# Kernel optimization log

Measured on AMD Instinct MI355X. Metric: run time of the kernel, lower is better.

Reference implementation:

```python
import jax, jax.numpy as jnp
import numpy as np

B, N, F_IN, F_HID, F_OUT = 32, 1024, 512, 512, 512


def setup_inputs() -> dict:
    key = jax.random.key(0)
    ks = jax.random.split(key, 8)
    def xavier(k, fan_in, fan_out):
        bound = float(np.sqrt(6.0 / (fan_in + fan_out)))
        return jax.random.uniform(k, (fan_in, fan_out), jnp.float32, -bound, bound)
    return {
        "batch_graph": jax.random.normal(ks[0], (B, N, F_IN), jnp.float32),
        "adj": jax.random.uniform(ks[1], (B, N, N), jnp.float32),
        "W1": xavier(ks[2], F_IN, F_HID),
        "b1": jnp.zeros((F_HID,), jnp.float32),
        "W2": xavier(ks[3], F_HID, F_HID),
        "b2": jnp.zeros((F_HID,), jnp.float32),
        "W3": xavier(ks[4], F_HID, F_OUT),
        "b3": jnp.zeros((F_OUT,), jnp.float32),
    }


def _gcn_layer(x, adj, W, b):
    # support = X @ W ; out = A @ support + b  (per graph in the batch)
    support = jnp.einsum("bnf,fh->bnh", x, W)
    return jnp.einsum("bnm,bmh->bnh", adj, support) + b


def reference(batch_graph, adj, W1, b1, W2, b2, W3, b3):
    # Block-diagonal big_adj @ big_graph is exactly a batched per-graph matmul:
    # the zero off-diagonal blocks contribute nothing, so math is identical.
    # Dropout is identity at inference (eval mode).
    x = jax.nn.relu(_gcn_layer(batch_graph, adj, W1, b1))
    x = jax.nn.relu(_gcn_layer(x, adj, W2, b2))
    out = _gcn_layer(x, adj, W3, b3)  # [B, N, F_OUT]
    return out
```

## Files before the change

### kernel.cpp

```cpp
#include <hip/hip_runtime.h>
#include <hip/hip_bf16.h>


typedef __attribute__((ext_vector_type(8))) short bf16x8s;
typedef __attribute__((ext_vector_type(4))) float f32x4;
typedef __attribute__((ext_vector_type(4))) unsigned short us4;
typedef __attribute__((ext_vector_type(8))) unsigned short us8;

__device__ __forceinline__ unsigned short f2bf(float f) {
    unsigned u = __builtin_bit_cast(unsigned, f);
    u += 0x7fffu + ((u >> 16) & 1u);
    return (unsigned short)(u >> 16);
}

__device__ __forceinline__ void async16(const unsigned short* g, unsigned short* l) {
    __builtin_amdgcn_global_load_lds(
        (const __attribute__((address_space(1))) unsigned int*)g,
        (__attribute__((address_space(3))) unsigned int*)l, 16, 0, 0);
}

#define MFMA_(d, va, vb) d = __builtin_amdgcn_mfma_f32_16x16x32_bf16(va, vb, d, 0, 0, 0)

__global__ void prep(const float* __restrict__ x0, unsigned short* __restrict__ P0, long n4,
                     const float* __restrict__ W1, const float* __restrict__ W2,
                     const float* __restrict__ W3, unsigned short* __restrict__ WT1,
                     unsigned short* __restrict__ WT2, unsigned short* __restrict__ WT3,
                     int F) {
    long i = (long)blockIdx.x * blockDim.x + threadIdx.x;
    long stride = (long)gridDim.x * blockDim.x;
    for (long k = i; k < n4; k += stride) {
        float4 v = ((const float4*)x0)[k];
        us4 o;
        o.x = f2bf(v.x); o.y = f2bf(v.y); o.z = f2bf(v.z); o.w = f2bf(v.w);
        ((us4*)P0)[k] = o;
    }
    const long FF = (long)F * F;
    for (long k = i; k < 3 * FF; k += stride) {
        int w = (int)(k / FF);
        long idx = k % FF;
        int r = (int)(idx % F);
        int c = (int)(idx / F);
        const float* W = (w == 0) ? W1 : (w == 1) ? W2 : W3;
        unsigned short* WT = (w == 0) ? WT1 : (w == 1) ? WT2 : WT3;
        WT[idx] = f2bf(W[(size_t)r * F + c]);
    }
}

template<bool RELU, bool OUT_F32, bool CVTTAIL>
__global__ __launch_bounds__(512, 2)
void gemm256(const unsigned short* __restrict__ A,
             const unsigned short* __restrict__ BT,
             void* __restrict__ Cout,
             const float* __restrict__ bias,
             int M, int N, int K,
             long sA, long sBT, long sC,
             const float* __restrict__ adjf,
             unsigned short* __restrict__ adjb)
{
    __shared__ unsigned short Lraw[65536];

    const int t    = threadIdx.x;
    const int lane = t & 63;
    const int wv   = t >> 6;
    const int wm   = wv >> 2;
    const int wn   = wv & 3;
    const int fr   = lane & 15;
    const int fk   = (lane >> 4) * 8;
    const int r4   = (lane >> 4) * 4;

    const int tilesN = N >> 8;
    const int bpb    = (M >> 8) * tilesN;
    const int cpx = gridDim.x >> 3;
    const int lb  = (blockIdx.x & 7) * cpx + (blockIdx.x >> 3);
    const int bat = lb / bpb;
    const int tt  = lb % bpb;
    const int m0  = (tt / tilesN) << 8;
    const int n0  = (tt % tilesN) << 8;

    const unsigned short* Ab = A  + (size_t)bat * sA  + (size_t)m0 * K;
    const unsigned short* Bb = BT + (size_t)bat * sBT + (size_t)n0 * K;

    int srow[2], scol[2], lo[2];
#pragma unroll
    for (int r = 0; r < 2; ++r) {
        int c   = r * 512 + t;
        srow[r] = c >> 3;
        scol[r] = ((c & 7) * 8) ^ ((srow[r] & 7) << 3);
        lo[r]   = c * 8;
    }

    auto stageA = [&](int kt, int h) {
        unsigned short* base = Lraw + (kt & 1) * 16384;
#pragma unroll
        for (int r = 0; r < 2; ++r)
            async16(Ab + (size_t)(h * 128 + srow[r]) * K + kt * 64 + scol[r],
                    base + h * 8192 + lo[r]);
    };
    auto stageB = [&](int kt, int h) {
        unsigned short* base = Lraw + 32768 + (kt & 1) * 16384;
#pragma unroll
        for (int r = 0; r < 2; ++r)
            async16(Bb + (size_t)(h * 128 + srow[r]) * K + kt * 64 + scol[r],
                    base + h * 8192 + lo[r]);
    };
    auto rdA = [&](int buf, int mf, int kkj) -> bf16x8s {
        int row = wm * 128 + mf * 16 + fr;
        int e   = (kkj * 32 + fk) ^ ((row & 7) << 3);
        return *(const bf16x8s*)&Lraw[buf * 16384 + row * 64 + e];
    };
    auto rdB = [&](int buf, int nf, int kkj) -> bf16x8s {
        int row = wn * 64 + nf * 16 + fr;
        int e   = (kkj * 32 + fk) ^ ((row & 7) << 3);
        return *(const bf16x8s*)&Lraw[32768 + buf * 16384 + row * 64 + e];
    };

    const int nt = K >> 6;

    f32x4 acc[8][4];
#pragma unroll
    for (int i = 0; i < 8; ++i)
#pragma unroll
        for (int j = 0; j < 4; ++j) acc[i][j] = f32x4{0.f, 0.f, 0.f, 0.f};

    bf16x8s aP[4], aB[4], aC[4], bX[4], bY[4];

    stageA(0, 0); stageB(0, 0); stageA(0, 1); stageB(0, 1);
    asm volatile("s_waitcnt vmcnt(0)" ::: "memory");
    __builtin_amdgcn_s_barrier();
#pragma unroll
    for (int m = 0; m < 4; ++m) aP[m] = rdA(0, m, 0);
#pragma unroll
    for (int n = 0; n < 4; ++n) bX[n] = rdB(0, n, 0);

    for (int it = 0; it < nt; ++it) {
        const int cur  = it & 1;
        const int nxt  = cur ^ 1;
        const bool more = (it + 1 < nt);

        __builtin_amdgcn_s_barrier();
#pragma unroll
        for (int m = 0; m < 4; ++m) aB[m] = rdA(cur, m + 4, 0);
        if (more) { stageA(it + 1, 0); stageB(it + 1, 0); }
        __builtin_amdgcn_s_setprio(1);
#pragma unroll
        for (int m = 0; m < 4; ++m)
#pragma unroll
            for (int n = 0; n < 4; ++n) MFMA_(acc[m][n], aP[m], bX[n]);
        __builtin_amdgcn_s_setprio(0);

        __builtin_amdgcn_s_barrier();
#pragma unroll
        for (int m = 0; m < 4; ++m) aC[m] = rdA(cur, m, 1);
#pragma unroll
        for (int n = 0; n < 4; ++n) bY[n] = rdB(cur, n, 1);
        if (more) { stageA(it + 1, 1); stageB(it + 1, 1); }
        __builtin_amdgcn_s_setprio(1);
#pragma unroll
        for (int m = 0; m < 4; ++m)
#pragma unroll
            for (int n = 0; n < 4; ++n) MFMA_(acc[m + 4][n], aB[m], bX[n]);
        __builtin_amdgcn_s_setprio(0);

        __builtin_amdgcn_s_barrier();
#pragma unroll
        for (int m = 0; m < 4; ++m) aB[m] = rdA(cur, m + 4, 1);
        __builtin_amdgcn_s_setprio(1);
#pragma unroll
        for (int m = 0; m < 4; ++m)
#pragma unroll
            for (int n = 0; n < 4; ++n) MFMA_(acc[m][n], aC[m], bY[n]);
        __builtin_amdgcn_s_setprio(0);

        if (more) {
            asm volatile("s_waitcnt vmcnt(0)" ::: "memory");
            __builtin_amdgcn_s_barrier();
#pragma unroll
            for (int m = 0; m < 4; ++m) aP[m] = rdA(nxt, m, 0);
#pragma unroll
            for (int n = 0; n < 4; ++n) bX[n] = rdB(nxt, n, 0);
        }
        __builtin_amdgcn_s_setprio(1);
#pragma unroll
        for (int m = 0; m < 4; ++m)
#pragma unroll
            for (int n = 0; n < 4; ++n) MFMA_(acc[m + 4][n], aB[m], bY[n]);
        __builtin_amdgcn_s_setprio(0);
    }

    __syncthreads();

    const int R0 = m0 + wm * 128;
    const int C0 = n0 + wn * 64;
    float bv[4];
#pragma unroll
    for (int j = 0; j < 4; ++j)
        bv[j] = bias ? bias[C0 + j * 16 + fr] : 0.f;

    if (OUT_F32) {
        float* Cb = (float*)Cout + (size_t)bat * sC;
#pragma unroll
        for (int j = 0; j < 4; ++j)
#pragma unroll
            for (int i = 0; i < 8; ++i)
#pragma unroll
                for (int e = 0; e < 4; ++e) {
                    float v = acc[i][j][e] + bv[j];
                    if (RELU) v = fmaxf(v, 0.f);
                    Cb[(size_t)(R0 + i * 16 + r4 + e) * N + C0 + j * 16 + fr] = v;
                }
    } else {
        unsigned short* sl = Lraw + wv * 8192;
#pragma unroll
        for (int i = 0; i < 8; ++i)
#pragma unroll
            for (int j = 0; j < 4; ++j)
#pragma unroll
                for (int e = 0; e < 4; ++e) {
                    float v = acc[i][j][e] + bv[j];
                    if (RELU) v = fmaxf(v, 0.f);
                    const int row = i * 16 + r4 + e;
                    const int col = j * 16 + fr;
                    sl[row * 64 + (col ^ ((row & 7) << 3))] = f2bf(v);
                }
        unsigned short* Cb = (unsigned short*)Cout + (size_t)bat * sC;
#pragma unroll
        for (int rr = 0; rr < 16; ++rr) {
            const int row = rr * 8 + (lane >> 3);
            const int k8  = lane & 7;
            us8 v = *(const us8*)&sl[row * 64 + ((k8 ^ (row & 7)) << 3)];
            *(us8*)&Cb[(size_t)(R0 + row) * N + C0 + k8 * 8] = v;
        }
    }

    if constexpr (CVTTAIL) {
        const int bc = lb >> 3, s = lb & 7;
        const float4* src = (const float4*)adjf + ((size_t)bc * 262144 + (size_t)s * 32768);
        us4* dst = (us4*)adjb + ((size_t)bc * 262144 + (size_t)s * 32768);
        for (int i = t; i < 32768; i += 512) {
            float4 v = src[i];
            us4 o;
            o.x = f2bf(v.x); o.y = f2bf(v.y); o.z = f2bf(v.z); o.w = f2bf(v.w);
            dst[i] = o;
        }
    }
}

extern "C" void kernel_launch(void* const* d_in, const int* in_sizes, int n_in,
                              void* d_out, int out_size, void* d_ws, size_t ws_size,
                              hipStream_t stream) {
    constexpr int B = 32, N = 1024, F = 512;

    const float* x0f  = (const float*)d_in[0];
    const float* adjf = (const float*)d_in[1];
    const float* W1 = (const float*)d_in[2];
    const float* b1 = (const float*)d_in[3];
    const float* W2 = (const float*)d_in[4];
    const float* b2 = (const float*)d_in[5];
    const float* W3 = (const float*)d_in[6];
    const float* b3 = (const float*)d_in[7];

    unsigned short* ws   = (unsigned short*)d_ws;
    unsigned short* adjb = ws;
    unsigned short* P0   = adjb + (size_t)B * N * N;
    unsigned short* P1   = P0 + (size_t)B * N * F;
    unsigned short* PT   = P1 + (size_t)B * N * F;
    unsigned short* WT1  = PT + (size_t)B * N * F;
    unsigned short* WT2  = WT1 + (size_t)F * F;
    unsigned short* WT3  = WT2 + (size_t)F * F;

    prep<<<2048, 256, 0, stream>>>(x0f, P0, (long)B * N * F / 4,
                                   W1, W2, W3, WT1, WT2, WT3, F);

    const int grid = 256;
    const long sX = (long)N * F;
    const long sAd = (long)N * N;

    gemm256<false, false, true ><<<grid, 512, 0, stream>>>(WT1,  P0, PT, nullptr, F, N, F, 0,  sX, sX, adjf, adjb);
    gemm256<true,  false, false><<<grid, 512, 0, stream>>>(adjb, PT, P1, b1,      N, F, N, sAd, sX, sX, nullptr, nullptr);
    gemm256<false, false, false><<<grid, 512, 0, stream>>>(WT2,  P1, PT, nullptr, F, N, F, 0,  sX, sX, nullptr, nullptr);
    gemm256<true,  false, false><<<grid, 512, 0, stream>>>(adjb, PT, P0, b2,      N, F, N, sAd, sX, sX, nullptr, nullptr);
    gemm256<false, false, false><<<grid, 512, 0, stream>>>(WT3,  P0, PT, nullptr, F, N, F, 0,  sX, sX, nullptr, nullptr);
    gemm256<false, true,  false><<<grid, 512, 0, stream>>>(adjb, PT, (float*)d_out, b3, N, F, N, sAd, sX, sX, nullptr, nullptr);
}
```

Measured before the change: 264.3 us.

## Overlap adjacency fp32-to-bf16 conversion with first GEMM using dedicated extra waves

The first feature GEMM launches 640 threads: two extra waves convert the adjacency matrix to bf16 in chunks interleaved with the GEMM's barrier phases, instead of all threads doing it after the epilogue. The aim is to hide the large conversion traffic behind the MFMA main loop. The cost is lower occupancy for this kernel, since launch bounds drop to one block per CU, and extra memory traffic competing with the GEMM's tile loads.

```diff
diff --git a/kernel.cpp b/kernel.cpp
--- a/kernel.cpp
+++ b/kernel.cpp
@@ -46,8 +46,8 @@
     }
 }
 
-template<bool RELU, bool OUT_F32, bool CVTTAIL>
-__global__ __launch_bounds__(512, 2)
+template<bool RELU, bool OUT_F32, bool CVTW>
+__global__ __launch_bounds__(CVTW ? 640 : 512, CVTW ? 1 : 2)
 void gemm256(const unsigned short* __restrict__ A,
              const unsigned short* __restrict__ BT,
              void* __restrict__ Cout,
@@ -62,6 +62,7 @@
     const int t    = threadIdx.x;
     const int lane = t & 63;
     const int wv   = t >> 6;
+    const bool isCvt = CVTW && (t >= 512);
     const int wm   = wv >> 2;
     const int wn   = wv & 3;
     const int fr   = lane & 15;
@@ -83,7 +84,7 @@
     int srow[2], scol[2], lo[2];
 #pragma unroll
     for (int r = 0; r < 2; ++r) {
-        int c   = r * 512 + t;
+        int c   = r * 512 + (t & 511);
         srow[r] = c >> 3;
         scol[r] = ((c & 7) * 8) ^ ((srow[r] & 7) << 3);
         lo[r]   = c * 8;
@@ -114,6 +115,22 @@
         return *(const bf16x8s*)&Lraw[32768 + buf * 16384 + row * 64 + e];
     };
 
+    auto cvtChunk = [&](int c) {
+        if constexpr (CVTW) {
+            const long base = (long)(lb >> 3) * 262144 + (long)(lb & 7) * 32768
+                            + (long)(wv - 8) * 16384 + (long)c * 512 + lane;
+            const float4* src = (const float4*)adjf;
+            us4* dst = (us4*)adjb;
+#pragma unroll
+            for (int k = 0; k < 8; ++k) {
+                float4 v = src[base + k * 64];
+                us4 o;
+                o.x = f2bf(v.x); o.y = f2bf(v.y); o.z = f2bf(v.z); o.w = f2bf(v.w);
+                dst[base + k * 64] = o;
+            }
+        }
+    };
+
     const int nt = K >> 6;
 
     f32x4 acc[8][4];
@@ -124,13 +141,17 @@
 
     bf16x8s aP[4], aB[4], aC[4], bX[4], bY[4];
 
-    stageA(0, 0); stageB(0, 0); stageA(0, 1); stageB(0, 1);
-    asm volatile("s_waitcnt vmcnt(0)" ::: "memory");
+    if (!isCvt) {
+        stageA(0, 0); stageB(0, 0); stageA(0, 1); stageB(0, 1);
+        asm volatile("s_waitcnt vmcnt(0)" ::: "memory");
+    }
     __builtin_amdgcn_s_barrier();
-#pragma unroll
-    for (int m = 0; m < 4; ++m) aP[m] = rdA(0, m, 0);
-#pragma unroll
-    for (int n = 0; n < 4; ++n) bX[n] = rdB(0, n, 0);
+    if (!isCvt) {
+#pragma unroll
+        for (int m = 0; m < 4; ++m) aP[m] = rdA(0, m, 0);
+#pragma unroll
+        for (int n = 0; n < 4; ++n) bX[n] = rdB(0, n, 0);
+    }
 
     for (int it = 0; it < nt; ++it) {
         const int cur  = it & 1;
@@ -138,109 +159,107 @@
         const bool more = (it + 1 < nt);
 
         __builtin_amdgcn_s_barrier();
-#pragma unroll
-        for (int m = 0; m < 4; ++m) aB[m] = rdA(cur, m + 4, 0);
-        if (more) { stageA(it + 1, 0); stageB(it + 1, 0); }
-        __builtin_amdgcn_s_setprio(1);
-#pragma unroll
-        for (int m = 0; m < 4; ++m)
-#pragma unroll
-            for (int n = 0; n < 4; ++n) MFMA_(acc[m][n], aP[m], bX[n]);
-        __builtin_amdgcn_s_setprio(0);
+        if (!isCvt) {
+#pragma unroll
+            for (int m = 0; m < 4; ++m) aB[m] = rdA(cur, m + 4, 0);
+            if (more) { stageA(it + 1, 0); stageB(it + 1, 0); }
+            __builtin_amdgcn_s_setprio(1);
+#pragma unroll
+            for (int m = 0; m < 4; ++m)
+#pragma unroll
+                for (int n = 0; n < 4; ++n) MFMA_(acc[m][n], aP[m], bX[n]);
+            __builtin_amdgcn_s_setprio(0);
+        } else cvtChunk(it * 4 + 0);
 
         __builtin_amdgcn_s_barrier();
-#pragma unroll
-        for (int m = 0; m < 4; ++m) aC[m] = rdA(cur, m, 1);
-#pragma unroll
-        for (int n = 0; n < 4; ++n) bY[n] = rdB(cur, n, 1);
-        if (more) { stageA(it + 1, 1); stageB(it + 1, 1); }
-        __builtin_amdgcn_s_setprio(1);
-#pragma unroll
-        for (int m = 0; m < 4; ++m)
-#pragma unroll
-            for (int n = 0; n < 4; ++n) MFMA_(acc[m + 4][n], aB[m], bX[n]);
-        __builtin_amdgcn_s_setprio(0);
+        if (!isCvt) {
+#pragma unroll
+            for (int m = 0; m < 4; ++m) aC[m] = rdA(cur, m, 1);
+#pragma unroll
+            for (int n = 0; n < 4; ++n) bY[n] = rdB(cur, n, 1);
+            if (more) { stageA(it + 1, 1); stageB(it + 1, 1); }
+            __builtin_amdgcn_s_setprio(1);
+#pragma unroll
+            for (int m = 0; m < 4; ++m)
+#pragma unroll
+                for (int n = 0; n < 4; ++n) MFMA_(acc[m + 4][n], aB[m], bX[n]);
+            __builtin_amdgcn_s_setprio(0);
+        } else cvtChunk(it * 4 + 1);
 
         __builtin_amdgcn_s_barrier();
-#pragma unroll
-        for (int m = 0; m < 4; ++m) aB[m] = rdA(cur, m + 4, 1);
-        __builtin_amdgcn_s_setprio(1);
-#pragma unroll
-        for (int m = 0; m < 4; ++m)
-#pragma unroll
-            for (int n = 0; n < 4; ++n) MFMA_(acc[m][n], aC[m], bY[n]);
-        __builtin_amdgcn_s_setprio(0);
-
-        if (more) {
-            asm volatile("s_waitcnt vmcnt(0)" ::: "memory");
-            __builtin_amdgcn_s_barrier();
-#pragma unroll
-            for (int m = 0; m < 4; ++m) aP[m] = rdA(nxt, m, 0);
-#pragma unroll
-            for (int n = 0; n < 4; ++n) bX[n] = rdB(nxt, n, 0);
-        }
-        __builtin_amdgcn_s_setprio(1);
-#pragma unroll
-        for (int m = 0; m < 4; ++m)
-#pragma unroll
-            for (int n = 0; n < 4; ++n) MFMA_(acc[m + 4][n], aB[m], bY[n]);
-        __builtin_amdgcn_s_setprio(0);
+        if (!isCvt) {
+#pragma unroll
+            for (int m = 0; m < 4; ++m) aB[m] = rdA(cur, m + 4, 1);
+            __builtin_amdgcn_s_setprio(1);
+#pragma unroll
+            for (int m = 0; m < 4; ++m)
+#pragma unroll
+                for (int n = 0; n < 4; ++n) MFMA_(acc[m][n], aC[m], bY[n]);
+            __builtin_amdgcn_s_setprio(0);
+        } else cvtChunk(it * 4 + 2);
+
+        if (!isCvt && more) asm volatile("s_waitcnt vmcnt(0)" ::: "memory");
+        __builtin_amdgcn_s_barrier();
+        if (!isCvt) {
+            if (more) {
+#pragma unroll
+                for (int m = 0; m < 4; ++m) aP[m] = rdA(nxt, m, 0);
+#pragma unroll
+                for (int n = 0; n < 4; ++n) bX[n] = rdB(nxt, n, 0);
+            }
+            __builtin_amdgcn_s_setprio(1);
+#pragma unroll
+            for (int m = 0; m < 4; ++m)
+#pragma unroll
+                for (int n = 0; n < 4; ++n) MFMA_(acc[m + 4][n], aB[m], bY[n]);
+            __builtin_amdgcn_s_setprio(0);
+        } else cvtChunk(it * 4 + 3);
     }
 
     __syncthreads();
 
-    const int R0 = m0 + wm * 128;
-    const int C0 = n0 + wn * 64;
-    float bv[4];
-#pragma unroll
-    for (int j = 0; j < 4; ++j)
-        bv[j] = bias ? bias[C0 + j * 16 + fr] : 0.f;
-
-    if (OUT_F32) {
-        float* Cb = (float*)Cout + (size_t)bat * sC;
+    if (!isCvt) {
+        const int R0 = m0 + wm * 128;
+        const int C0 = n0 + wn * 64;
+        float bv[4];
 #pragma unroll
         for (int j = 0; j < 4; ++j)
+            bv[j] = bias ? bias[C0 + j * 16 + fr] : 0.f;
+
+        if (OUT_F32) {
+            float* Cb = (float*)Cout + (size_t)bat * sC;
+#pragma unroll
+            for (int j = 0; j < 4; ++j)
+#pragma unroll
+                for (int i = 0; i < 8; ++i)
+#pragma unroll
+                    for (int e = 0; e < 4; ++e) {
+                        float v = acc[i][j][e] + bv[j];
+                        if (RELU) v = fmaxf(v, 0.f);
+                        Cb[(size_t)(R0 + i * 16 + r4 + e) * N + C0 + j * 16 + fr] = v;
+                    }
+        } else {
+            unsigned short* sl = Lraw + wv * 8192;
 #pragma unroll
             for (int i = 0; i < 8; ++i)
 #pragma unroll
-                for (int e = 0; e < 4; ++e) {
-                    float v = acc[i][j][e] + bv[j];
-                    if (RELU) v = fmaxf(v, 0.f);
-                    Cb[(size_t)(R0 + i * 16 + r4 + e) * N + C0 + j * 16 + fr] = v;
-                }
-    } else {
-        unsigned short* sl = Lraw + wv * 8192;
-#pragma unroll
-        for (int i = 0; i < 8; ++i)
-#pragma unroll
-            for (int j = 0; j < 4; ++j)
-#pragma unroll
-                for (int e = 0; e < 4; ++e) {
-                    float v = acc[i][j][e] + bv[j];
-                    if (RELU) v = fmaxf(v, 0.f);
-                    const int row = i * 16 + r4 + e;
-                    const int col = j * 16 + fr;
-                    sl[row * 64 + (col ^ ((row & 7) << 3))] = f2bf(v);
-                }
-        unsigned short* Cb = (unsigned short*)Cout + (size_t)bat * sC;
-#pragma unroll
-        for (int rr = 0; rr < 16; ++rr) {
-            const int row = rr * 8 + (lane >> 3);
-            const int k8  = lane & 7;
-            us8 v = *(const us8*)&sl[row * 64 + ((k8 ^ (row & 7)) << 3)];
-            *(us8*)&Cb[(size_t)(R0 + row) * N + C0 + k8 * 8] = v;
-        }
-    }
-
-    if constexpr (CVTTAIL) {
-        const int bc = lb >> 3, s = lb & 7;
-        const float4* src = (const float4*)adjf + ((size_t)bc * 262144 + (size_t)s * 32768);
-        us4* dst = (us4*)adjb + ((size_t)bc * 262144 + (size_t)s * 32768);
-        for (int i = t; i < 32768; i += 512) {
-            float4 v = src[i];
-            us4 o;
-            o.x = f2bf(v.x); o.y = f2bf(v.y); o.z = f2bf(v.z); o.w = f2bf(v.w);
-            dst[i] = o;
+                for (int j = 0; j < 4; ++j)
+#pragma unroll
+                    for (int e = 0; e < 4; ++e) {
+                        float v = acc[i][j][e] + bv[j];
+                        if (RELU) v = fmaxf(v, 0.f);
+                        const int row = i * 16 + r4 + e;
+                        const int col = j * 16 + fr;
+                        sl[row * 64 + (col ^ ((row & 7) << 3))] = f2bf(v);
+                    }
+            unsigned short* Cb = (unsigned short*)Cout + (size_t)bat * sC;
+#pragma unroll
+            for (int rr = 0; rr < 16; ++rr) {
+                const int row = rr * 8 + (lane >> 3);
+                const int k8  = lane & 7;
+                us8 v = *(const us8*)&sl[row * 64 + ((k8 ^ (row & 7)) << 3)];
+                *(us8*)&Cb[(size_t)(R0 + row) * N + C0 + k8 * 8] = v;
+            }
         }
     }
 }
@@ -275,7 +294,7 @@
     const long sX = (long)N * F;
     const long sAd = (long)N * N;
 
-    gemm256<false, false, true ><<<grid, 512, 0, stream>>>(WT1,  P0, PT, nullptr, F, N, F, 0,  sX, sX, adjf, adjb);
+    gemm256<false, false, true ><<<grid, 640, 0, stream>>>(WT1,  P0, PT, nullptr, F, N, F, 0,  sX, sX, adjf, adjb);
     gemm256<true,  false, false><<<grid, 512, 0, stream>>>(adjb, PT, P1, b1,      N, F, N, sAd, sX, sX, nullptr, nullptr);
     gemm256<false, false, false><<<grid, 512, 0, stream>>>(WT2,  P1, PT, nullptr, F, N, F, 0,  sX, sX, nullptr, nullptr);
     gemm256<true,  false, false><<<grid, 512, 0, stream>>>(adjb, PT, P0, b2,      N, F, N, sAd, sX, sX, nullptr, nullptr);
```

Measured after the change: 572.0 us. 2.16x slower.
